# Kernel optimization log

Measured on AMD Instinct MI355X. Metric: run time of the kernel, lower is better.

The kernel has to match this reference:

```python
import jax, jax.numpy as jnp
import numpy as np

NUM_HEADS = 8
NUM_KV_HEADS = 4
HEAD_DIM = 256
HIDDEN = 2048
SEQ = 4096
CHUNK_START = 2048
CHUNK_END = 4096
SOFTCAP = 50.0
EPS = 1e-6
ROPE_THETA = 10000.0
NEG_INF = -1e9


def _rms_norm(x, w, eps=EPS):
    # Gemma RMSNorm: computed in fp32, scale is (1 + w)
    x32 = x.astype(jnp.float32)
    out = x32 * jax.lax.rsqrt(jnp.mean(x32 * x32, axis=-1, keepdims=True) + eps)
    return (out * (1.0 + w.astype(jnp.float32))).astype(x.dtype)


def _rotate_half(x):
    h = x.shape[-1] // 2
    return jnp.concatenate([-x[..., h:], x[..., :h]], axis=-1)


def _apply_rope(x, cos, sin):
    # x: [B, S, H, D]; cos/sin: [B, S, D] -> unsqueeze head dim
    cos = cos[:, :, None, :]
    sin = sin[:, :, None, :]
    return x * cos + _rotate_half(x) * sin


def setup_inputs() -> dict:
    key = jax.random.key(0)
    ks = jax.random.split(key, 8)
    hidden_states = jax.random.normal(ks[0], (1, SEQ, HIDDEN), dtype=jnp.float32)
    # real RoPE tables
    inv_freq = 1.0 / (ROPE_THETA ** (np.arange(0, HEAD_DIM, 2, dtype=np.float32) / HEAD_DIM))
    pos = np.arange(SEQ, dtype=np.float32)
    freqs = np.outer(pos, inv_freq)                      # [S, D/2]
    emb = np.concatenate([freqs, freqs], axis=-1)        # [S, D]
    cos = jnp.asarray(np.cos(emb))[None]                 # [1, S, D]
    sin = jnp.asarray(np.sin(emb))[None]
    # causal additive mask for the chunk: query i (abs pos start+i) attends keys j <= start+i
    q_pos = np.arange(CHUNK_START, CHUNK_END)[:, None]
    k_pos = np.arange(CHUNK_END)[None, :]
    attention_mask = jnp.asarray(np.where(k_pos <= q_pos, 0.0, NEG_INF).astype(np.float32))[None, None]
    s = 0.02
    wq = jax.random.normal(ks[1], (HIDDEN, NUM_HEADS * HEAD_DIM), dtype=jnp.float32) * s
    wk = jax.random.normal(ks[2], (HIDDEN, NUM_KV_HEADS * HEAD_DIM), dtype=jnp.float32) * s
    wv = jax.random.normal(ks[3], (HIDDEN, NUM_KV_HEADS * HEAD_DIM), dtype=jnp.float32) * s
    wo = jax.random.normal(ks[4], (NUM_HEADS * HEAD_DIM, HIDDEN), dtype=jnp.float32) * s
    q_norm_w = jnp.zeros((HEAD_DIM,), dtype=jnp.float32)
    k_norm_w = jnp.zeros((HEAD_DIM,), dtype=jnp.float32)
    v_norm_w = jnp.zeros((HEAD_DIM,), dtype=jnp.float32)
    return {
        'hidden_states': hidden_states, 'cos': cos, 'sin': sin,
        'attention_mask': attention_mask,
        'wq': wq, 'wk': wk, 'wv': wv, 'wo': wo,
        'q_norm_w': q_norm_w, 'k_norm_w': k_norm_w, 'v_norm_w': v_norm_w,
        'start': CHUNK_START, 'end': CHUNK_END,
    }


def reference(hidden_states, cos, sin, attention_mask, wq, wk, wv, wo,
              q_norm_w, k_norm_w, v_norm_w, start, end):
    B = hidden_states.shape[0]
    chunk = end - start
    scaling = HEAD_DIM ** -0.5

    # ---- queries from the chunk ----
    q = (hidden_states[:, start:end] @ wq).reshape(B, chunk, NUM_HEADS, HEAD_DIM)
    q = _rms_norm(q, q_norm_w)
    q = _apply_rope(q, cos[:, start:end], sin[:, start:end])
    q = q.transpose(0, 2, 1, 3)                         # [B, H, chunk, D]

    # ---- keys / values over [0, end) ----
    kv_h = hidden_states[:, :end]
    k = (kv_h @ wk).reshape(B, end, NUM_KV_HEADS, HEAD_DIM)
    k = _rms_norm(k, k_norm_w)
    k = _apply_rope(k, cos[:, :end], sin[:, :end]).transpose(0, 2, 1, 3)   # [B, KV, end, D]
    v = (kv_h @ wv).reshape(B, end, NUM_KV_HEADS, HEAD_DIM)
    v = _rms_norm(v, v_norm_w).transpose(0, 2, 1, 3)                        # [B, KV, end, D]

    # ---- GQA repeat_kv ----
    n_rep = NUM_HEADS // NUM_KV_HEADS
    k = jnp.repeat(k, n_rep, axis=1)                    # [B, H, end, D]
    v = jnp.repeat(v, n_rep, axis=1)

    # ---- eager attention with logit softcap ----
    logits = jnp.einsum('bhqd,bhkd->bhqk', q, k) * scaling
    logits = jnp.tanh(logits / SOFTCAP) * SOFTCAP
    logits = logits + attention_mask
    attn = jax.nn.softmax(logits.astype(jnp.float32), axis=-1).astype(q.dtype)
    out = jnp.einsum('bhqk,bhkd->bhqd', attn, v)
    out = out.transpose(0, 2, 1, 3).reshape(B, chunk, NUM_HEADS * HEAD_DIM)
    return out @ wo
```

## Files before the change

kernel.cpp:

```cpp
#include <hip/hip_runtime.h>

#define HID 2048
#define SEQL 4096
#define CHUNK 2048
#define NHEADS 8
#define NKVH 4
#define HDIM 256

typedef __bf16 bf16x4 __attribute__((ext_vector_type(4)));
typedef __bf16 bf16x8 __attribute__((ext_vector_type(8)));
typedef float f32x4 __attribute__((ext_vector_type(4)));
typedef _Float16 f16x4 __attribute__((ext_vector_type(4)));
typedef __attribute__((address_space(1))) unsigned int* as1_u32;
typedef __attribute__((address_space(3))) unsigned int* as3_u32;

__device__ __forceinline__ void load_lds16(const __bf16* g, __bf16* l) {
  __builtin_amdgcn_global_load_lds((as1_u32)g, (as3_u32)l, 16, 0, 0);
}

__global__ void cvt_bf16_kernel(const float* __restrict__ X, __bf16* __restrict__ Y) {
  int i = blockIdx.x * blockDim.x + threadIdx.x;
  const float4* xv = (const float4*)X;
  float4 v = xv[i];
  bf16x4 o;
  o[0] = (__bf16)v.x; o[1] = (__bf16)v.y; o[2] = (__bf16)v.z; o[3] = (__bf16)v.w;
  *(bf16x4*)(Y + i * 4) = o;
}

__global__ void transpose_all_kernel(const float* __restrict__ wq, const float* __restrict__ wk,
                                     const float* __restrict__ wv, const float* __restrict__ wo,
                                     __bf16* __restrict__ WQT, __bf16* __restrict__ WKVT,
                                     __bf16* __restrict__ WOT) {
  __shared__ float tile[64][65];
  const int b = blockIdx.x;
  const float* W;
  __bf16* WT;
  int R, C, bx, by;
  if (b < 1024) { W = wq; WT = WQT; R = 2048; C = 2048; bx = b & 31; by = b >> 5; }
  else if (b < 1536) { int q = b - 1024; W = wk; WT = WKVT; R = 2048; C = 1024; bx = q & 15; by = q >> 4; }
  else if (b < 2048) { int q = b - 1536; W = wv; WT = WKVT + (size_t)1024 * 2048; R = 2048; C = 1024; bx = q & 15; by = q >> 4; }
  else { int q = b - 2048; W = wo; WT = WOT; R = 2048; C = 2048; bx = q & 31; by = q >> 5; }
  int r0 = by * 64, c0 = bx * 64;
  for (int i = threadIdx.x; i < 4096; i += 256) {
    int r = i >> 6, c = i & 63;
    tile[r][c] = W[(size_t)(r0 + r) * C + c0 + c];
  }
  __syncthreads();
  for (int i = threadIdx.x; i < 4096; i += 256) {
    int c = i >> 6, r = i & 63;
    WT[(size_t)(c0 + c) * R + r0 + r] = (__bf16)tile[r][c];
  }
}

__global__ __launch_bounds__(256, 3) void proj_kernel(
    const __bf16* __restrict__ Xb, const __bf16* __restrict__ WQT,
    const __bf16* __restrict__ WKVT, __bf16* __restrict__ Qp, __bf16* __restrict__ KVp) {
  __shared__ __bf16 Asm[2][128 * 32];
  __shared__ __bf16 Bsm[2][128 * 32];
  const int tid = threadIdx.x;
  const int lane = tid & 63, wave = tid >> 6;
  const int quad = lane >> 4, l15 = lane & 15;
  const int b = blockIdx.x;
  const __bf16 *A, *B;
  __bf16* C;
  int m0, n0;
  if (b < 512) {
    A = Xb; B = WKVT; C = KVp;
    m0 = (b & 31) * 128; n0 = (b >> 5) * 128;
  } else {
    int q = b - 512;
    A = Xb + (size_t)2048 * 2048; B = WQT; C = Qp;
    m0 = (q & 15) * 128; n0 = (q >> 4) * 128;
  }
  const int wm = (wave & 1) * 64, wn = (wave >> 1) * 64;
  f32x4 acc[4][4];
#pragma unroll
  for (int i = 0; i < 4; i++)
#pragma unroll
    for (int j = 0; j < 4; j++) acc[i][j] = (f32x4){0.f, 0.f, 0.f, 0.f};

  const int rA = lane >> 2, cA = (lane & 3) * 8;

#pragma unroll
  for (int c = wave; c < 8; c += 4) {
    load_lds16(A + (size_t)(m0 + c * 16 + rA) * 2048 + cA, &Asm[0][c * 512]);
    load_lds16(B + (size_t)(n0 + c * 16 + rA) * 2048 + cA, &Bsm[0][c * 512]);
  }

  for (int k0 = 0; k0 < 2048; k0 += 32) {
    const int buf = (k0 >> 5) & 1;
    __syncthreads();
    if (k0 + 32 < 2048) {
#pragma unroll
      for (int c = wave; c < 8; c += 4) {
        load_lds16(A + (size_t)(m0 + c * 16 + rA) * 2048 + k0 + 32 + cA, &Asm[buf ^ 1][c * 512]);
        load_lds16(B + (size_t)(n0 + c * 16 + rA) * 2048 + k0 + 32 + cA, &Bsm[buf ^ 1][c * 512]);
      }
    }
    bf16x8 af[4], bfr[4];
#pragma unroll
    for (int i = 0; i < 4; i++) {
      af[i] = *(const bf16x8*)(&Asm[buf][(wm + i * 16 + l15) * 32 + quad * 8]);
      bfr[i] = *(const bf16x8*)(&Bsm[buf][(wn + i * 16 + l15) * 32 + quad * 8]);
    }
#pragma unroll
    for (int mi = 0; mi < 4; mi++)
#pragma unroll
      for (int ni = 0; ni < 4; ni++)
        acc[mi][ni] = __builtin_amdgcn_mfma_f32_16x16x32_bf16(af[mi], bfr[ni], acc[mi][ni], 0, 0, 0);
  }
#pragma unroll
  for (int mi = 0; mi < 4; mi++) {
    int r = m0 + wm + mi * 16 + quad * 4;
#pragma unroll
    for (int ni = 0; ni < 4; ni++) {
      int cc = n0 + wn + ni * 16 + l15;
#pragma unroll
      for (int j = 0; j < 4; j++)
        C[(size_t)(r + j) * 2048 + cc] = (__bf16)acc[mi][ni][j];
    }
  }
}

template <int NI, bool F32OUT>
__global__ __launch_bounds__(256, 2) void gemm_bt_kernel(
    const __bf16* __restrict__ A, const __bf16* __restrict__ B,
    void* __restrict__ Cv, int M, int N, int Kd) {
  constexpr int BN = NI * 32;
  __shared__ __bf16 Asm[2][128 * 32];
  __shared__ __bf16 Bsm[2][BN * 32];
  const int tid = threadIdx.x;
  const int lane = tid & 63, wave = tid >> 6;
  const int quad = lane >> 4, l15 = lane & 15;
  const int m0 = blockIdx.x * 128, n0 = blockIdx.y * BN;
  const int wm = (wave & 1) * 64, wn = (wave >> 1) * (NI * 16);
  f32x4 acc[4][NI];
#pragma unroll
  for (int i = 0; i < 4; i++)
#pragma unroll
    for (int j = 0; j < NI; j++) acc[i][j] = (f32x4){0.f, 0.f, 0.f, 0.f};

  const int rA = lane >> 2, cA = (lane & 3) * 8;

#pragma unroll
  for (int c = wave; c < 8; c += 4)
    load_lds16(A + (size_t)(m0 + c * 16 + rA) * Kd + cA, &Asm[0][c * 512]);
#pragma unroll
  for (int c = wave; c < BN / 16; c += 4)
    load_lds16(B + (size_t)(n0 + c * 16 + rA) * Kd + cA, &Bsm[0][c * 512]);

  for (int k0 = 0; k0 < Kd; k0 += 32) {
    const int buf = (k0 >> 5) & 1;
    __syncthreads();
    if (k0 + 32 < Kd) {
#pragma unroll
      for (int c = wave; c < 8; c += 4)
        load_lds16(A + (size_t)(m0 + c * 16 + rA) * Kd + k0 + 32 + cA, &Asm[buf ^ 1][c * 512]);
#pragma unroll
      for (int c = wave; c < BN / 16; c += 4)
        load_lds16(B + (size_t)(n0 + c * 16 + rA) * Kd + k0 + 32 + cA, &Bsm[buf ^ 1][c * 512]);
    }
    bf16x8 af[4], bfr[NI];
#pragma unroll
    for (int i = 0; i < 4; i++)
      af[i] = *(const bf16x8*)(&Asm[buf][(wm + i * 16 + l15) * 32 + quad * 8]);
#pragma unroll
    for (int i = 0; i < NI; i++)
      bfr[i] = *(const bf16x8*)(&Bsm[buf][(wn + i * 16 + l15) * 32 + quad * 8]);
#pragma unroll
    for (int mi = 0; mi < 4; mi++)
#pragma unroll
      for (int ni = 0; ni < NI; ni++)
        acc[mi][ni] = __builtin_amdgcn_mfma_f32_16x16x32_bf16(af[mi], bfr[ni], acc[mi][ni], 0, 0, 0);
  }
#pragma unroll
  for (int mi = 0; mi < 4; mi++) {
    int r = m0 + wm + mi * 16 + quad * 4;
#pragma unroll
    for (int ni = 0; ni < NI; ni++) {
      int cc = n0 + wn + ni * 16 + l15;
#pragma unroll
      for (int j = 0; j < 4; j++) {
        if (F32OUT)
          ((float*)Cv)[(size_t)(r + j) * N + cc] = acc[mi][ni][j];
        else
          ((__bf16*)Cv)[(size_t)(r + j) * N + cc] = (__bf16)acc[mi][ni][j];
      }
    }
  }
}

__global__ void norm_all_kernel(__bf16* __restrict__ Qp, __bf16* __restrict__ KVp,
                                __bf16* __restrict__ VT,
                                const float* __restrict__ cosb, const float* __restrict__ sinb,
                                const float* __restrict__ qw, const float* __restrict__ kw,
                                const float* __restrict__ vw) {
  const int gw = (blockIdx.x * 256 + threadIdx.x) >> 6;
  const int lane = threadIdx.x & 63;
  const int d0 = lane * 4;

  __bf16* row;
  const float* w;
  int pos = -1;
  int vh = 0, vt = 0;
  bool isV = false;
  float prescale = 1.f;
  if (gw < 16384) {
    int t = gw >> 3, h = gw & 7;
    row = Qp + (size_t)t * 2048 + h * 256;
    w = qw; pos = t + 2048; prescale = 0.0625f;
  } else {
    int g2 = gw - 16384;
    int t = g2 >> 3, r = g2 & 7;
    if (r < 4) {
      row = KVp + (size_t)t * 2048 + r * 256;
      w = kw; pos = t;
    } else {
      row = KVp + (size_t)t * 2048 + 1024 + (r - 4) * 256;
      w = vw; isV = true; vh = r - 4; vt = t;
    }
  }

  bf16x4 rv = *(const bf16x4*)(row + d0);
  float x[4];
  float ss = 0.f;
#pragma unroll
  for (int j = 0; j < 4; j++) { x[j] = (float)rv[j]; ss += x[j] * x[j]; }
#pragma unroll
  for (int off = 1; off < 64; off <<= 1) ss += __shfl_xor(ss, off);
  float scale = rsqrtf(ss * (1.f / 256.f) + 1e-6f);
  float n[4];
#pragma unroll
  for (int j = 0; j < 4; j++) n[j] = x[j] * scale * (1.f + w[d0 + j]);

  if (!isV) {
    const float* cp = cosb + (size_t)pos * 256 + d0;
    const float* sp = sinb + (size_t)pos * 256 + d0;
    bf16x4 ov;
#pragma unroll
    for (int j = 0; j < 4; j++) {
      float other = __shfl_xor(n[j], 32);
      float rot = (lane < 32) ? -other : other;
      ov[j] = (__bf16)((n[j] * cp[j] + rot * sp[j]) * prescale);
    }
    *(bf16x4*)(row + d0) = ov;
  } else {
#pragma unroll
    for (int j = 0; j < 4; j++)
      VT[(size_t)vh * (256 * 4096) + (size_t)(d0 + j) * 4096 + vt] = (__bf16)n[j];
  }
}

__global__ __launch_bounds__(256, 2) void attn_kernel(
    const __bf16* __restrict__ Q,
    const __bf16* __restrict__ K,
    const __bf16* __restrict__ VT,
    _Float16* __restrict__ Op,
    float* __restrict__ Lp) {
  __shared__ __bf16 Ksm[2][8][32][32];
  __shared__ __bf16 Vsm[2][256][32];
  __shared__ __bf16 Pex[4][32][40];
  const int tid = threadIdx.x;
  const int lane = tid & 63, wave = tid >> 6;
  const int quad = lane >> 4, l15 = lane & 15;
  const int b = blockIdx.x;
  const int idx = b & 255;
  const int h = idx & 7, sp = (idx >> 3) & 3;
  int qt = idx >> 5;
  if (b >= 256) qt = 15 - qt;
  const int kvh = h >> 1;

  const int T = 68 + 4 * qt;
  const int nst = T >> 2;

  bf16x8 qf[2][8];
#pragma unroll
  for (int r = 0; r < 2; r++) {
    const __bf16* qp = Q + (size_t)(qt * 128 + wave * 32 + r * 16 + l15) * 2048 + h * 256 + quad * 8;
#pragma unroll
    for (int s = 0; s < 8; s++) qf[r][s] = *(const bf16x8*)(qp + s * 32);
  }
  f32x4 o[2][16];
#pragma unroll
  for (int r = 0; r < 2; r++)
#pragma unroll
    for (int i = 0; i < 16; i++) o[r][i] = (f32x4){0.f, 0.f, 0.f, 0.f};
  float rs[2][4] = {{0.f, 0.f, 0.f, 0.f}, {0.f, 0.f, 0.f, 0.f}};

  const __bf16* Kb = K + kvh * 256;
  const __bf16* Vb = VT + (size_t)kvh * (256 * 4096);
  const int rA = lane >> 2;
  const int cAs = (((lane & 3) ^ ((rA >> 1) & 3)) * 8);
  const int kx = (quad ^ ((l15 >> 1) & 3)) * 8;
  const int qbase = 2048 + qt * 128 + wave * 32 + quad * 4;

  {
    const int t0 = sp * 32;
#pragma unroll
    for (int ch = 0; ch < 4; ch++) {
      int cc = wave + ch * 4;
      int s = cc >> 1, hf = cc & 1;
      load_lds16(Kb + (size_t)(t0 + hf * 16 + rA) * 2048 + s * 32 + cAs, &Ksm[0][s][hf * 16][0]);
      load_lds16(Vb + (size_t)(cc * 16 + rA) * 4096 + t0 + cAs, &Vsm[0][cc * 16][0]);
    }
  }

  for (int i = 0; i < nst; i++) {
    const int buf = i & 1;
    const int t0 = (4 * i + sp) * 32;
    __syncthreads();
    if (i + 1 < nst) {
      const int t1 = t0 + 128;
#pragma unroll
      for (int ch = 0; ch < 4; ch++) {
        int cc = wave + ch * 4;
        int s = cc >> 1, hf = cc & 1;
        load_lds16(Kb + (size_t)(t1 + hf * 16 + rA) * 2048 + s * 32 + cAs, &Ksm[buf ^ 1][s][hf * 16][0]);
        load_lds16(Vb + (size_t)(cc * 16 + rA) * 4096 + t1 + cAs, &Vsm[buf ^ 1][cc * 16][0]);
      }
    }

    f32x4 s4[2][2];
    s4[0][0] = (f32x4){0.f, 0.f, 0.f, 0.f};
    s4[0][1] = s4[0][0]; s4[1][0] = s4[0][0]; s4[1][1] = s4[0][0];
#pragma unroll
    for (int s = 0; s < 8; s++) {
      bf16x8 b0 = *(const bf16x8*)(&Ksm[buf][s][l15][kx]);
      bf16x8 b1 = *(const bf16x8*)(&Ksm[buf][s][16 + l15][kx]);
      s4[0][0] = __builtin_amdgcn_mfma_f32_16x16x32_bf16(qf[0][s], b0, s4[0][0], 0, 0, 0);
      s4[0][1] = __builtin_amdgcn_mfma_f32_16x16x32_bf16(qf[0][s], b1, s4[0][1], 0, 0, 0);
      s4[1][0] = __builtin_amdgcn_mfma_f32_16x16x32_bf16(qf[1][s], b0, s4[1][0], 0, 0, 0);
      s4[1][1] = __builtin_amdgcn_mfma_f32_16x16x32_bf16(qf[1][s], b1, s4[1][1], 0, 0, 0);
    }

    const bool mk = (i == nst - 1);
#pragma unroll
    for (int r = 0; r < 2; r++)
#pragma unroll
      for (int nt = 0; nt < 2; nt++) {
        const int key = t0 + nt * 16 + l15;
#pragma unroll
        for (int j = 0; j < 4; j++) {
          float v = s4[r][nt][j];
          float e = __expf(v * 0.04f);
          float p = __expf(-100.f * __builtin_amdgcn_rcpf(e + 1.f));
          if (mk && key > qbase + r * 16 + j) p = 0.f;
          s4[r][nt][j] = p;
          rs[r][j] += p;
        }
      }

#pragma unroll
    for (int r = 0; r < 2; r++)
#pragma unroll
      for (int nt = 0; nt < 2; nt++)
#pragma unroll
        for (int j = 0; j < 4; j++)
          Pex[wave][r * 16 + quad * 4 + j][nt * 16 + l15] = (__bf16)s4[r][nt][j];

    bf16x8 pf0 = *(const bf16x8*)(&Pex[wave][l15][quad * 8]);
    bf16x8 pf1 = *(const bf16x8*)(&Pex[wave][16 + l15][quad * 8]);
#pragma unroll
    for (int d = 0; d < 16; d++) {
      bf16x8 vf = *(const bf16x8*)(&Vsm[buf][d * 16 + l15][kx]);
      o[0][d] = __builtin_amdgcn_mfma_f32_16x16x32_bf16(pf0, vf, o[0][d], 0, 0, 0);
      o[1][d] = __builtin_amdgcn_mfma_f32_16x16x32_bf16(pf1, vf, o[1][d], 0, 0, 0);
    }
  }

#pragma unroll
  for (int off = 1; off < 16; off <<= 1)
#pragma unroll
    for (int r = 0; r < 2; r++)
#pragma unroll
      for (int j = 0; j < 4; j++) rs[r][j] += __shfl_xor(rs[r][j], off);

  _Float16* Os = Op + (size_t)sp * (2048 * 2048);
  float* Ls = Lp + sp * (2048 * 8);
#pragma unroll
  for (int r = 0; r < 2; r++) {
    float inv[4];
#pragma unroll
    for (int j = 0; j < 4; j++)
      inv[j] = rs[r][j] > 0.f ? 1.f / rs[r][j] : 0.f;
    const int trow = qt * 128 + wave * 32 + r * 16 + quad * 4;
#pragma unroll
    for (int d = 0; d < 16; d++) {
      const int col = h * 256 + d * 16 + l15;
#pragma unroll
      for (int j = 0; j < 4; j++)
        Os[(size_t)(trow + j) * 2048 + col] = (_Float16)(o[r][d][j] * inv[j]);
    }
    if (l15 == 0) {
#pragma unroll
      for (int j = 0; j < 4; j++) Ls[(trow + j) * 8 + h] = rs[r][j];
    }
  }
}

__global__ void merge_kernel(const _Float16* __restrict__ Op, const float* __restrict__ Lp,
                             __bf16* __restrict__ AO) {
  int f = (blockIdx.x * 256 + threadIdx.x) * 4;
  int q = f >> 11, col = f & 2047, h = col >> 8;
  float lsum = 0.f;
  float acc[4] = {0.f, 0.f, 0.f, 0.f};
#pragma unroll
  for (int s = 0; s < 4; s++) {
    float l = Lp[s * (2048 * 8) + q * 8 + h];
    lsum += l;
    f16x4 v = *(const f16x4*)(Op + (size_t)s * (2048 * 2048) + f);
#pragma unroll
    for (int j = 0; j < 4; j++) acc[j] += l * (float)v[j];
  }
  float inv = 1.f / lsum;
  bf16x4 o;
#pragma unroll
  for (int j = 0; j < 4; j++) o[j] = (__bf16)(acc[j] * inv);
  *(bf16x4*)(AO + f) = o;
}

extern "C" void kernel_launch(void* const* d_in, const int* in_sizes, int n_in,
                              void* d_out, int out_size, void* d_ws, size_t ws_size,
                              hipStream_t stream) {
  const float* hidden = (const float*)d_in[0];
  const float* cosb = (const float*)d_in[1];
  const float* sinb = (const float*)d_in[2];
  const float* wq = (const float*)d_in[4];
  const float* wk = (const float*)d_in[5];
  const float* wv = (const float*)d_in[6];
  const float* wo = (const float*)d_in[7];
  const float* qw = (const float*)d_in[8];
  const float* kw = (const float*)d_in[9];
  const float* vw = (const float*)d_in[10];
  float* outp = (float*)d_out;

  char* p = (char*)d_ws;
  __bf16* Xb = (__bf16*)p;   p += (size_t)SEQL * HID * 2;
  __bf16* WQT = (__bf16*)p;  p += (size_t)2048 * 2048 * 2;
  __bf16* WKVT = (__bf16*)p; p += (size_t)2048 * 2048 * 2;
  __bf16* WOT = (__bf16*)p;  p += (size_t)2048 * 2048 * 2;
  __bf16* Qp = (__bf16*)p;   p += (size_t)2048 * 2048 * 2;
  __bf16* KVp = (__bf16*)p;  p += (size_t)4096 * 2048 * 2;
  __bf16* VT = (__bf16*)p;   p += (size_t)4 * 256 * 4096 * 2;
  __bf16* AO = (__bf16*)p;   p += (size_t)2048 * 2048 * 2;
  float* Lpart = (float*)p;  p += (size_t)4 * 2048 * 8 * 4;
  _Float16* Opart = (_Float16*)Xb;

  cvt_bf16_kernel<<<8192, 256, 0, stream>>>(hidden, Xb);
  transpose_all_kernel<<<3072, 256, 0, stream>>>(wq, wk, wv, wo, WQT, WKVT, WOT);

  proj_kernel<<<768, 256, 0, stream>>>(Xb, WQT, WKVT, Qp, KVp);

  norm_all_kernel<<<12288, 256, 0, stream>>>(Qp, KVp, VT, cosb, sinb, qw, kw, vw);

  attn_kernel<<<512, 256, 0, stream>>>(Qp, KVp, VT, Opart, Lpart);
  merge_kernel<<<4096, 256, 0, stream>>>(Opart, Lpart, AO);

  gemm_bt_kernel<2, true><<<dim3(16, 32), 256, 0, stream>>>(AO, WOT, outp, 2048, 2048, 2048);
}
```

Before: 389.1 us.

## Replace projection GEMM with 256x256-tile 8-wave kernel and split out V transpose

Measured after the change: 379.6 us. 1.03x faster.

```diff
diff --git a/kernel.cpp b/kernel.cpp
--- a/kernel.cpp
+++ b/kernel.cpp
@@ -52,74 +52,142 @@
   }
 }
 
-__global__ __launch_bounds__(256, 3) void proj_kernel(
-    const __bf16* __restrict__ Xb, const __bf16* __restrict__ WQT,
-    const __bf16* __restrict__ WKVT, __bf16* __restrict__ Qp, __bf16* __restrict__ KVp) {
-  __shared__ __bf16 Asm[2][128 * 32];
-  __shared__ __bf16 Bsm[2][128 * 32];
+template <int MODE>
+__global__ __launch_bounds__(512, 2) void gemm256_kernel(
+    const __bf16* __restrict__ A0, const __bf16* __restrict__ B0,
+    const __bf16* __restrict__ B1, void* __restrict__ C0, void* __restrict__ C1) {
+  __shared__ __bf16 Asm[2][256 * 64];
+  __shared__ __bf16 Bsm[2][256 * 64];
   const int tid = threadIdx.x;
   const int lane = tid & 63, wave = tid >> 6;
   const int quad = lane >> 4, l15 = lane & 15;
-  const int b = blockIdx.x;
+  const int wm = (wave & 1) * 128, wn = (wave >> 1) * 64;
+
   const __bf16 *A, *B;
-  __bf16* C;
+  char* Cb;
   int m0, n0;
-  if (b < 512) {
-    A = Xb; B = WKVT; C = KVp;
-    m0 = (b & 31) * 128; n0 = (b >> 5) * 128;
+  if (MODE == 0) {
+    int b = blockIdx.x;
+    if (b < 128) { A = A0; B = B0; Cb = (char*)C0; m0 = (b & 15) * 256; n0 = (b >> 4) * 256; }
+    else { int q = b - 128; A = A0 + (size_t)2048 * 2048; B = B1; Cb = (char*)C1; m0 = (q & 7) * 256; n0 = (q >> 3) * 256; }
   } else {
-    int q = b - 512;
-    A = Xb + (size_t)2048 * 2048; B = WQT; C = Qp;
-    m0 = (q & 15) * 128; n0 = (q >> 4) * 128;
-  }
-  const int wm = (wave & 1) * 64, wn = (wave >> 1) * 64;
-  f32x4 acc[4][4];
-#pragma unroll
-  for (int i = 0; i < 4; i++)
+    A = A0; B = B0; Cb = (char*)C0;
+    m0 = (int)(blockIdx.x & 7) * 256; n0 = (int)(blockIdx.x >> 3) * 256;
+  }
+
+  f32x4 acc[8][4];
+#pragma unroll
+  for (int i = 0; i < 8; i++)
 #pragma unroll
     for (int j = 0; j < 4; j++) acc[i][j] = (f32x4){0.f, 0.f, 0.f, 0.f};
 
-  const int rA = lane >> 2, cA = (lane & 3) * 8;
-
-#pragma unroll
-  for (int c = wave; c < 8; c += 4) {
-    load_lds16(A + (size_t)(m0 + c * 16 + rA) * 2048 + cA, &Asm[0][c * 512]);
-    load_lds16(B + (size_t)(n0 + c * 16 + rA) * 2048 + cA, &Bsm[0][c * 512]);
-  }
-
-  for (int k0 = 0; k0 < 2048; k0 += 32) {
-    const int buf = (k0 >> 5) & 1;
-    __syncthreads();
-    if (k0 + 32 < 2048) {
-#pragma unroll
-      for (int c = wave; c < 8; c += 4) {
-        load_lds16(A + (size_t)(m0 + c * 16 + rA) * 2048 + k0 + 32 + cA, &Asm[buf ^ 1][c * 512]);
-        load_lds16(B + (size_t)(n0 + c * 16 + rA) * 2048 + k0 + 32 + cA, &Bsm[buf ^ 1][c * 512]);
+  const int rr = tid >> 3;
+  const int gch = (tid & 7) ^ ((tid >> 3) & 7);
+  const int ldsb = wave * 512;
+
+  const int sx = l15 & 7;
+  const int s0 = ((0 + quad) ^ sx) * 8;
+  const int s1 = ((4 + quad) ^ sx) * 8;
+
+#define STAGE(T, BF)                                                                  \
+  {                                                                                   \
+    const int k0s = (T) * 64;                                                         \
+    _Pragma("unroll")                                                                 \
+    for (int a = 0; a < 4; a++) {                                                     \
+      load_lds16(A + (size_t)(m0 + a * 64 + rr) * 2048 + k0s + gch * 8,               \
+                 &Asm[BF][a * 4096 + ldsb]);                                          \
+      load_lds16(B + (size_t)(n0 + a * 64 + rr) * 2048 + k0s + gch * 8,               \
+                 &Bsm[BF][a * 4096 + ldsb]);                                          \
+    }                                                                                 \
+  }
+
+#define LDA(MH, BF)                                                                   \
+  _Pragma("unroll")                                                                   \
+  for (int mi = 0; mi < 4; mi++) {                                                    \
+    const int rowb = (wm + (MH) * 64 + mi * 16 + l15) * 64;                           \
+    af[mi * 2 + 0] = *(const bf16x8*)(&Asm[BF][rowb + s0]);                           \
+    af[mi * 2 + 1] = *(const bf16x8*)(&Asm[BF][rowb + s1]);                           \
+  }
+
+#define LDB(DST, NH, BF)                                                              \
+  _Pragma("unroll")                                                                   \
+  for (int ni = 0; ni < 2; ni++) {                                                    \
+    const int rowb = (wn + (NH) * 32 + ni * 16 + l15) * 64;                           \
+    DST[ni * 2 + 0] = *(const bf16x8*)(&Bsm[BF][rowb + s0]);                          \
+    DST[ni * 2 + 1] = *(const bf16x8*)(&Bsm[BF][rowb + s1]);                          \
+  }
+
+#define MMA(MH, NH, BV)                                                               \
+  __builtin_amdgcn_s_setprio(1);                                                      \
+  _Pragma("unroll")                                                                   \
+  for (int mi = 0; mi < 4; mi++)                                                      \
+    _Pragma("unroll")                                                                 \
+    for (int ni = 0; ni < 2; ni++) {                                                  \
+      acc[(MH) * 4 + mi][(NH) * 2 + ni] = __builtin_amdgcn_mfma_f32_16x16x32_bf16(    \
+          af[mi * 2 + 0], BV[ni * 2 + 0], acc[(MH) * 4 + mi][(NH) * 2 + ni], 0, 0, 0);\
+      acc[(MH) * 4 + mi][(NH) * 2 + ni] = __builtin_amdgcn_mfma_f32_16x16x32_bf16(    \
+          af[mi * 2 + 1], BV[ni * 2 + 1], acc[(MH) * 4 + mi][(NH) * 2 + ni], 0, 0, 0);\
+    }                                                                                 \
+  __builtin_amdgcn_s_setprio(0);
+
+  bf16x8 af[8], bX[4], bY[4];
+
+  STAGE(0, 0);
+  STAGE(1, 1);
+  asm volatile("s_waitcnt vmcnt(8)" ::: "memory");
+  __builtin_amdgcn_s_barrier();
+
+  const int NT = 32;
+#pragma unroll 2
+  for (int t = 0; t < NT; t++) {
+    const int c = t & 1;
+    LDA(0, c); LDB(bX, 0, c);
+    __builtin_amdgcn_s_barrier();
+    MMA(0, 0, bX);
+    __builtin_amdgcn_s_barrier();
+    LDB(bY, 1, c);
+    __builtin_amdgcn_s_barrier();
+    MMA(0, 1, bY);
+    __builtin_amdgcn_s_barrier();
+    LDA(1, c);
+    __builtin_amdgcn_s_barrier();
+    MMA(1, 1, bY);
+    __builtin_amdgcn_s_barrier();
+    LDB(bX, 0, c);
+    __builtin_amdgcn_s_barrier();
+    MMA(1, 0, bX);
+    __builtin_amdgcn_s_barrier();
+    if (t + 2 < NT) {
+      STAGE(t + 2, c);
+      asm volatile("s_waitcnt vmcnt(8)" ::: "memory");
+      __builtin_amdgcn_s_barrier();
+    } else if (t + 1 < NT) {
+      asm volatile("s_waitcnt vmcnt(0)" ::: "memory");
+      __builtin_amdgcn_s_barrier();
+    }
+  }
+
+#pragma unroll
+  for (int mh = 0; mh < 2; mh++)
+#pragma unroll
+    for (int mi = 0; mi < 4; mi++) {
+      const int r = m0 + wm + mh * 64 + mi * 16 + quad * 4;
+#pragma unroll
+      for (int ni = 0; ni < 4; ni++) {
+        const int cc = n0 + wn + (ni >> 1) * 32 + (ni & 1) * 16 + l15;
+#pragma unroll
+        for (int j = 0; j < 4; j++) {
+          if (MODE == 1)
+            ((float*)Cb)[(size_t)(r + j) * 2048 + cc] = acc[mh * 4 + mi][ni][j];
+          else
+            ((__bf16*)Cb)[(size_t)(r + j) * 2048 + cc] = (__bf16)acc[mh * 4 + mi][ni][j];
+        }
       }
     }
-    bf16x8 af[4], bfr[4];
-#pragma unroll
-    for (int i = 0; i < 4; i++) {
-      af[i] = *(const bf16x8*)(&Asm[buf][(wm + i * 16 + l15) * 32 + quad * 8]);
-      bfr[i] = *(const bf16x8*)(&Bsm[buf][(wn + i * 16 + l15) * 32 + quad * 8]);
-    }
-#pragma unroll
-    for (int mi = 0; mi < 4; mi++)
-#pragma unroll
-      for (int ni = 0; ni < 4; ni++)
-        acc[mi][ni] = __builtin_amdgcn_mfma_f32_16x16x32_bf16(af[mi], bfr[ni], acc[mi][ni], 0, 0, 0);
-  }
-#pragma unroll
-  for (int mi = 0; mi < 4; mi++) {
-    int r = m0 + wm + mi * 16 + quad * 4;
-#pragma unroll
-    for (int ni = 0; ni < 4; ni++) {
-      int cc = n0 + wn + ni * 16 + l15;
-#pragma unroll
-      for (int j = 0; j < 4; j++)
-        C[(size_t)(r + j) * 2048 + cc] = (__bf16)acc[mi][ni][j];
-    }
-  }
+#undef STAGE
+#undef LDA
+#undef LDB
+#undef MMA
 }
 
 template <int NI, bool F32OUT>
@@ -191,7 +259,6 @@
 }
 
 __global__ void norm_all_kernel(__bf16* __restrict__ Qp, __bf16* __restrict__ KVp,
-                                __bf16* __restrict__ VT,
                                 const float* __restrict__ cosb, const float* __restrict__ sinb,
                                 const float* __restrict__ qw, const float* __restrict__ kw,
                                 const float* __restrict__ vw) {
@@ -202,7 +269,6 @@
   __bf16* row;
   const float* w;
   int pos = -1;
-  int vh = 0, vt = 0;
   bool isV = false;
   float prescale = 1.f;
   if (gw < 16384) {
@@ -217,7 +283,7 @@
       w = kw; pos = t;
     } else {
       row = KVp + (size_t)t * 2048 + 1024 + (r - 4) * 256;
-      w = vw; isV = true; vh = r - 4; vt = t;
+      w = vw; isV = true;
     }
   }
 
@@ -245,9 +311,37 @@
     }
     *(bf16x4*)(row + d0) = ov;
   } else {
-#pragma unroll
-    for (int j = 0; j < 4; j++)
-      VT[(size_t)vh * (256 * 4096) + (size_t)(d0 + j) * 4096 + vt] = (__bf16)n[j];
+    bf16x4 ov;
+#pragma unroll
+    for (int j = 0; j < 4; j++) ov[j] = (__bf16)n[j];
+    *(bf16x4*)(row + d0) = ov;
+  }
+}
+
+__global__ void vtrans_kernel(const __bf16* __restrict__ KVp, __bf16* __restrict__ VT) {
+  __shared__ __bf16 tile[64][72];
+  const int b = blockIdx.x;
+  const int h = b >> 8;
+  const int r = b & 255;
+  const int t0 = (r >> 2) * 64;
+  const int d0 = (r & 3) * 64;
+  const __bf16* src = KVp + 1024 + h * 256 + d0;
+#pragma unroll
+  for (int it = 0; it < 2; it++) {
+    int idx = it * 256 + threadIdx.x;
+    int tt = idx >> 3, dd = (idx & 7) * 8;
+    *(bf16x8*)(&tile[tt][dd]) = *(const bf16x8*)(src + (size_t)(t0 + tt) * 2048 + dd);
+  }
+  __syncthreads();
+  __bf16* dst = VT + (size_t)h * (256 * 4096) + (size_t)d0 * 4096 + t0;
+#pragma unroll
+  for (int it = 0; it < 2; it++) {
+    int idx = it * 256 + threadIdx.x;
+    int dd = idx >> 3, tt = (idx & 7) * 8;
+    bf16x8 o;
+#pragma unroll
+    for (int j = 0; j < 8; j++) o[j] = tile[tt + j][dd];
+    *(bf16x8*)(dst + (size_t)dd * 4096 + tt) = o;
   }
 }
 
@@ -449,9 +543,10 @@
   cvt_bf16_kernel<<<8192, 256, 0, stream>>>(hidden, Xb);
   transpose_all_kernel<<<3072, 256, 0, stream>>>(wq, wk, wv, wo, WQT, WKVT, WOT);
 
-  proj_kernel<<<768, 256, 0, stream>>>(Xb, WQT, WKVT, Qp, KVp);
-
-  norm_all_kernel<<<12288, 256, 0, stream>>>(Qp, KVp, VT, cosb, sinb, qw, kw, vw);
+  gemm256_kernel<0><<<192, 512, 0, stream>>>(Xb, WKVT, WQT, KVp, Qp);
+
+  norm_all_kernel<<<12288, 256, 0, stream>>>(Qp, KVp, cosb, sinb, qw, kw, vw);
+  vtrans_kernel<<<1024, 256, 0, stream>>>(KVp, VT);
 
   attn_kernel<<<512, 256, 0, stream>>>(Qp, KVp, VT, Opart, Lpart);
   merge_kernel<<<4096, 256, 0, stream>>>(Opart, Lpart, AO);
```
